# Optimization experiments

Measured on AMD Instinct MI355X. Metric: run time of the kernel, lower is better.

The kernel has to match this reference:

```python
import jax, jax.numpy as jnp
import numpy as np

HID = 64
IN_DIM = 6


def setup_inputs() -> dict:
    key = jax.random.key(0)
    ks = jax.random.split(key, 16)
    B, S, N, D = 8, 32, 64, IN_DIM
    g = lambda k, shape, fan_in: jax.random.normal(k, shape, jnp.float32) / np.sqrt(fan_in)
    return {
        "x": jax.random.normal(ks[0], (B, S, N, D), jnp.float32),
        "emb_w": g(ks[1], (D, HID), D),
        "emb_b": jnp.zeros((HID,), jnp.float32),
        "edge_w1": g(ks[2], (2 * HID + 1, HID), 2 * HID + 1),
        "edge_b1": jnp.zeros((HID,), jnp.float32),
        "edge_w2": g(ks[3], (HID, HID), HID),
        "edge_b2": jnp.zeros((HID,), jnp.float32),
        "node_w1": g(ks[4], (2 * HID, HID), 2 * HID),
        "node_b1": jnp.zeros((HID,), jnp.float32),
        "node_w2": g(ks[5], (HID, HID), HID),
        "node_b2": jnp.zeros((HID,), jnp.float32),
        "coord_w1": g(ks[6], (HID, HID), HID),
        "coord_b1": jnp.zeros((HID,), jnp.float32),
        "coord_w2": g(ks[7], (HID, 1), HID),
        "final_w": g(ks[8], (HID, IN_DIM), HID),
        "final_b": jnp.zeros((IN_DIM,), jnp.float32),
    }


def reference(x, emb_w, emb_b, edge_w1, edge_b1, edge_w2, edge_b2,
              node_w1, node_b1, node_w2, node_b2,
              coord_w1, coord_b1, coord_w2, final_w, final_b):
    B, S, N, D = x.shape
    xf = x.reshape(B * S, N, D)           # [G,N,6]
    pos, vel = xf[..., :3], xf[..., 3:]
    h = xf @ emb_w + emb_b                # [G,N,H]

    rel = pos[:, :, None, :] - pos[:, None, :, :]          # [G,N,N,3]
    dist_sq = jnp.sum(rel * rel, axis=-1, keepdims=True)   # [G,N,N,1]

    H = h.shape[-1]
    h_i = jnp.broadcast_to(h[:, :, None, :], (B * S, N, N, H))
    h_j = jnp.broadcast_to(h[:, None, :, :], (B * S, N, N, H))
    e_in = jnp.concatenate([h_i, h_j, dist_sq], axis=-1)   # [G,N,N,2H+1]
    m_ij = jax.nn.relu(e_in @ edge_w1 + edge_b1) @ edge_w2 + edge_b2  # [G,N,N,H]
    m_i = m_ij.sum(axis=2)                                  # [G,N,H]

    w = jax.nn.relu(m_ij @ coord_w1 + coord_b1) @ coord_w2  # [G,N,N,1]
    pos_out = pos + (rel * w).sum(axis=2) / N

    n_in = jnp.concatenate([h, m_i], axis=-1)
    h = h + jax.nn.relu(n_in @ node_w1 + node_b1) @ node_w2 + node_b2
    vel_out = vel + (h @ final_w + final_b)[..., 3:]

    out = jnp.concatenate([pos_out, vel_out], axis=-1)
    return out.reshape(B, S, N, D)
```

## Files before the change

### kernel.cpp

```cpp
#include <hip/hip_runtime.h>


#define NG 256

typedef __attribute__((ext_vector_type(4))) float f32x4;
typedef __attribute__((ext_vector_type(8))) __bf16 bf16x8;

__device__ __forceinline__ f32x4 mfma16(bf16x8 a, bf16x8 b, f32x4 c){
  return __builtin_amdgcn_mfma_f32_16x16x32_bf16(a, b, c, 0, 0, 0);
}

__device__ __forceinline__ void fma4x4(float* acc, float4 a, float4 b){
  acc[0]  += a.x*b.x; acc[1]  += a.x*b.y; acc[2]  += a.x*b.z; acc[3]  += a.x*b.w;
  acc[4]  += a.y*b.x; acc[5]  += a.y*b.y; acc[6]  += a.y*b.z; acc[7]  += a.y*b.w;
  acc[8]  += a.z*b.x; acc[9]  += a.z*b.y; acc[10] += a.z*b.z; acc[11] += a.z*b.w;
  acc[12] += a.w*b.x; acc[13] += a.w*b.y; acc[14] += a.w*b.z; acc[15] += a.w*b.w;
}

__global__ __launch_bounds__(512, 1)
void egnn_edge_mfma(const float* __restrict__ x,
    const float* __restrict__ emb_w,  const float* __restrict__ emb_b,
    const float* __restrict__ edge_w1,const float* __restrict__ edge_b1,
    const float* __restrict__ edge_w2,const float* __restrict__ edge_b2,
    const float* __restrict__ coord_w1,const float* __restrict__ coord_b1,
    const float* __restrict__ coord_w2,
    float* __restrict__ out, float* __restrict__ ws_mi)
{
  __shared__ __align__(16) float  sAB [64*64];
  __shared__ __align__(16) __bf16 sC  [64*72];
  __shared__ __align__(16) __bf16 sW3t[64*72];
  __shared__ __align__(16) __bf16 sW2t[64*72];
  __shared__ __align__(16) __bf16 sTr [64*72];
  __shared__ float sDsq[8][64];
  __shared__ float sPX[64], sPY[64], sPZ[64];
  __shared__ __align__(16) float sW1L[64];
  __shared__ float sCB1p[64], sCW2[64], sB2[64], sB1[64];
  __shared__ __align__(16) float sW1a[64*64], sW1b[64*64], sW2T[64*64], sCW1[64*64];
  __shared__ __align__(16) float sHt[64*64];
  __shared__ float sXL[384], sEW[384], sEB[64];

  const int bs  = blockIdx.x, tid = threadIdx.x;
  const int lane = tid & 63, wv = tid >> 6;
  const float* xg = x + bs*384;

  if (tid < 384){ sXL[tid] = xg[tid]; sEW[tid] = emb_w[tid]; }
  if (tid < 64){
    sEB[tid] = emb_b[tid];  sB1[tid] = edge_b1[tid]; sB2[tid] = edge_b2[tid];
    sCW2[tid] = coord_w2[tid]; sW1L[tid] = edge_w1[128*64 + tid];
  } else if (tid < 128){
    int j = tid-64; sPX[j]=xg[j*6]; sPY[j]=xg[j*6+1]; sPZ[j]=xg[j*6+2];
  }
  {
    const float4* w1 = (const float4*)edge_w1;
    const float4* cw = (const float4*)coord_w1;
    float4* da=(float4*)sW1a; float4* db=(float4*)sW1b; float4* dc=(float4*)sCW1;
    #pragma unroll
    for (int e=0;e<2;e++){ int q=tid+e*512; da[q]=w1[q]; db[q]=w1[1024+q]; dc[q]=cw[q]; }
  }
  #pragma unroll
  for (int e=0;e<8;e++){ int idx=tid+e*512; int n=idx>>6, k=idx&63;
    sW2T[idx] = edge_w2[k*64+n]; }
  __syncthreads();

  #pragma unroll
  for (int e=0;e<8;e++){
    int idx=tid+e*512; int m=idx>>6, j=idx&63;
    float v = sEB[m];
    #pragma unroll
    for (int d=0;d<6;d++) v += sXL[j*6+d]*sEW[d*64+m];
    sHt[idx] = v;
  }
  __syncthreads();

  const int g = tid>>8, tl = tid&255, tjx = tl>>4, tnx = tl&15;
  {
    float acc[16] = {};
    const float* Bm = g ? sW1b : sW1a;
    #pragma unroll 8
    for (int k=0;k<64;k++){
      float4 av = *(const float4*)&sHt[k*64 + 4*tjx];
      float4 bv = *(const float4*)&Bm [k*64 + 4*tnx];
      fma4x4(acc, av, bv);
    }
    if (g==0){
      #pragma unroll
      for (int r=0;r<4;r++)
        #pragma unroll
        for (int c=0;c<4;c++)
          sAB[(4*tjx+r)*64 + 4*tnx+c] = acc[r*4+c] + sB1[4*tnx+c];
    } else {
      #pragma unroll
      for (int r=0;r<4;r++)
        #pragma unroll
        for (int c=0;c<4;c++)
          sC[(4*tjx+r)*72 + 4*tnx+c] = (__bf16)acc[r*4+c];
    }
  }
  if (g==0){
    float acc[16] = {};
    #pragma unroll 8
    for (int k=0;k<64;k++){
      float4 av = *(const float4*)&sW2T[k*64 + 4*tjx];
      float4 bv = *(const float4*)&sCW1[k*64 + 4*tnx];
      fma4x4(acc, av, bv);
    }
    #pragma unroll
    for (int r=0;r<4;r++)
      #pragma unroll
      for (int c=0;c<4;c++)
        sW3t[(4*tnx+c)*72 + 4*tjx+r] = (__bf16)acc[r*4+c];
  } else {
    #pragma unroll
    for (int e=0;e<16;e++){ int idx=tl+e*256; sW2t[(idx>>6)*72 + (idx&63)] = (__bf16)sW2T[idx]; }
    if (tl < 64){
      float s = coord_b1[tl];
      for (int n=0;n<64;n++) s += sB2[n]*sCW1[n*64+tl];
      sCB1p[tl] = s;
    }
  }
  __syncthreads();

  const int lg = lane>>4, ln = lane&15;

  bf16x8 bW3[4][2];
  #pragma unroll
  for (int nt=0;nt<4;nt++)
    #pragma unroll
    for (int kb=0;kb<2;kb++)
      bW3[nt][kb] = *(const bf16x8*)&sW3t[(nt*16+ln)*72 + kb*32 + lg*8];
  float w18[2][8];
  #pragma unroll
  for (int kb=0;kb<2;kb++){
    *(float4*)&w18[kb][0] = *(const float4*)&sW1L[kb*32+lg*8];
    *(float4*)&w18[kb][4] = *(const float4*)&sW1L[kb*32+lg*8+4];
  }
  float cb1v[4], cw2v[4];
  #pragma unroll
  for (int nt=0;nt<4;nt++){ cb1v[nt]=sCB1p[nt*16+ln]; cw2v[nt]=sCW2[nt*16+ln]; }

  for (int ib=0; ib<8; ib++){
    const int i = ib*8 + wv;
    {
      float dx=sPX[i]-sPX[lane], dy=sPY[i]-sPY[lane], dz=sPZ[i]-sPZ[lane];
      sDsq[wv][lane] = dx*dx+dy*dy+dz*dz;
    }
    float ab8[2][8];
    #pragma unroll
    for (int kb=0;kb<2;kb++){
      *(float4*)&ab8[kb][0] = *(const float4*)&sAB[i*64 + kb*32+lg*8];
      *(float4*)&ab8[kb][4] = *(const float4*)&sAB[i*64 + kb*32+lg*8+4];
    }
    float trs[2][8];
    #pragma unroll
    for (int kb=0;kb<2;kb++)
      #pragma unroll
      for (int e=0;e<8;e++) trs[kb][e]=0.f;

    float sw=0.f, swx=0.f, swy=0.f, swz=0.f;

    #pragma unroll
    for (int jt=0;jt<4;jt++){
      const int j = jt*16 + ln;
      const float dq = sDsq[wv][j];
      f32x4 a4[4];
      #pragma unroll
      for (int nt=0;nt<4;nt++) a4[nt] = f32x4{0.f,0.f,0.f,0.f};

      #pragma unroll
      for (int kb=0;kb<2;kb++){
        bf16x8 c8 = *(const bf16x8*)&sC[j*72 + kb*32 + lg*8];
        bf16x8 t8;
        #pragma unroll
        for (int e=0;e<8;e++){
          float v = ab8[kb][e] + (float)c8[e] + dq*w18[kb][e];
          v = fmaxf(v, 0.f);
          trs[kb][e] += v;
          t8[e] = (__bf16)v;
        }
        #pragma unroll
        for (int nt=0;nt<4;nt++)
          a4[nt] = mfma16(t8, bW3[nt][kb], a4[nt]);
      }

      float wr[4];
      #pragma unroll
      for (int r=0;r<4;r++){
        float p = 0.f;
        #pragma unroll
        for (int nt=0;nt<4;nt++){
          float u = a4[nt][r] + cb1v[nt];
          p += fmaxf(u, 0.f)*cw2v[nt];
        }
        p += __shfl_xor(p,1); p += __shfl_xor(p,2);
        p += __shfl_xor(p,4); p += __shfl_xor(p,8);
        wr[r] = p;
      }
      #pragma unroll
      for (int r=0;r<4;r++){
        int jj = jt*16 + lg*4 + r;
        sw  += wr[r];
        swx += wr[r]*sPX[jj];
        swy += wr[r]*sPY[jj];
        swz += wr[r]*sPZ[jj];
      }
    }

    #pragma unroll
    for (int kb=0;kb<2;kb++)
      #pragma unroll
      for (int e=0;e<8;e++){
        float s = trs[kb][e];
        s += __shfl_xor(s,1); s += __shfl_xor(s,2);
        s += __shfl_xor(s,4); s += __shfl_xor(s,8);
        trs[kb][e] = s;
      }
    if (ln == 0){
      #pragma unroll
      for (int kb=0;kb<2;kb++){
        bf16x8 t8;
        #pragma unroll
        for (int e=0;e<8;e++) t8[e] = (__bf16)trs[kb][e];
        *(bf16x8*)&sTr[i*72 + kb*32 + lg*8] = t8;
      }
    }

    sw  += __shfl_xor(sw,16);  sw  += __shfl_xor(sw,32);
    swx += __shfl_xor(swx,16); swx += __shfl_xor(swx,32);
    swy += __shfl_xor(swy,16); swy += __shfl_xor(swy,32);
    swz += __shfl_xor(swz,16); swz += __shfl_xor(swz,32);
    if (lane == 0){
      float* o = out + (bs*64 + i)*6;
      o[0] = sPX[i] + (sPX[i]*sw - swx)*(1.f/64.f);
      o[1] = sPY[i] + (sPY[i]*sw - swy)*(1.f/64.f);
      o[2] = sPZ[i] + (sPZ[i]*sw - swz)*(1.f/64.f);
    }
  }

  __syncthreads();
  #pragma unroll
  for (int t2=0;t2<2;t2++){
    int t  = wv*2 + t2;
    int it = t>>2, nt = t&3;
    f32x4 a2 = f32x4{0.f,0.f,0.f,0.f};
    #pragma unroll
    for (int kb=0;kb<2;kb++){
      bf16x8 a8 = *(const bf16x8*)&sTr [(it*16+ln)*72 + kb*32 + lg*8];
      bf16x8 b8 = *(const bf16x8*)&sW2t[(nt*16+ln)*72 + kb*32 + lg*8];
      a2 = mfma16(a8, b8, a2);
    }
    int n = nt*16 + ln;
    float b2n = 64.f*sB2[n];
    #pragma unroll
    for (int r=0;r<4;r++){
      int i = it*16 + lg*4 + r;
      ws_mi[(bs*64 + i)*64 + n] = a2[r] + b2n;
    }
  }
}

__global__ __launch_bounds__(256)
void egnn_node_kernel(const float* __restrict__ x,
    const float* __restrict__ emb_w,  const float* __restrict__ emb_b,
    const float* __restrict__ node_w1,const float* __restrict__ node_b1,
    const float* __restrict__ node_w2,const float* __restrict__ node_b2,
    const float* __restrict__ final_w,const float* __restrict__ final_b,
    float* __restrict__ out, const float* __restrict__ ws_mi)
{
  __shared__ __align__(16) float sHt [64*64];
  __shared__ __align__(16) float sMIt[64*68];
  __shared__ __align__(16) float sNW1[128*64];
  __shared__ __align__(16) float sNW2[64*64];
  __shared__ __align__(16) float sZt [64*68];
  __shared__ float sXL[384], sEW[384], sEB[64], sNB1[64], sNB2[64];
  __shared__ float sFW[64*3], sFB[3];

  const int bs = blockIdx.x, tid = threadIdx.x;
  const float* xg = x + bs*64*6;

  for (int q=tid; q<384; q+=256){ sXL[q]=xg[q]; sEW[q]=emb_w[q]; }
  if (tid < 64){ sEB[tid]=emb_b[tid]; sNB1[tid]=node_b1[tid]; sNB2[tid]=node_b2[tid]; }
  if (tid < 192) sFW[tid] = final_w[(tid/3)*6 + 3 + (tid%3)];
  if (tid < 3)   sFB[tid] = final_b[3+tid];
  {
    const float4* g1 = (const float4*)node_w1; float4* d1 = (float4*)sNW1;
    #pragma unroll
    for (int e=0;e<8;e++) d1[tid + e*256] = g1[tid + e*256];
    const float4* g2 = (const float4*)node_w2; float4* d2 = (float4*)sNW2;
    #pragma unroll
    for (int e=0;e<4;e++) d2[tid + e*256] = g2[tid + e*256];
  }
  const float* mig = ws_mi + bs*4096;
  #pragma unroll
  for (int e=0;e<16;e++){
    int idx = tid + e*256; int iN = idx>>6, n = idx&63;
    sMIt[n*68 + iN] = mig[idx];
  }
  __syncthreads();
  #pragma unroll
  for (int e=0;e<16;e++){
    int idx = tid + e*256; int m = idx>>6, j = idx&63;
    float v = sEB[m];
    #pragma unroll
    for (int d=0;d<6;d++) v += sXL[j*6+d]*sEW[d*64+m];
    sHt[idx] = v;
  }
  __syncthreads();

  const int tj = tid>>4, tn = tid&15;
  {
    float acc[16] = {};
    #pragma unroll 8
    for (int k=0;k<64;k++){
      float4 av = *(const float4*)&sHt [k*64 + 4*tj];
      float4 bv = *(const float4*)&sNW1[k*64 + 4*tn];
      fma4x4(acc, av, bv);
    }
    #pragma unroll 8
    for (int k=0;k<64;k++){
      float4 av = *(const float4*)&sMIt[k*68 + 4*tj];
      float4 bv = *(const float4*)&sNW1[(64+k)*64 + 4*tn];
      fma4x4(acc, av, bv);
    }
    #pragma unroll
    for (int c=0;c<4;c++){
      float nb = sNB1[4*tn+c];
      float4 v = make_float4(fmaxf(acc[0+c]+nb,0.f), fmaxf(acc[4+c]+nb,0.f),
                             fmaxf(acc[8+c]+nb,0.f), fmaxf(acc[12+c]+nb,0.f));
      *(float4*)&sZt[(4*tn+c)*68 + 4*tj] = v;
    }
  }
  __syncthreads();
  {
    float acc[16] = {};
    #pragma unroll 8
    for (int k=0;k<64;k++){
      float4 av = *(const float4*)&sZt [k*68 + 4*tj];
      float4 bv = *(const float4*)&sNW2[k*64 + 4*tn];
      fma4x4(acc, av, bv);
    }
    float fv[4][3] = {};
    #pragma unroll
    for (int r=0;r<4;r++){
      #pragma unroll
      for (int c=0;c<4;c++){
        int n = 4*tn+c, j = 4*tj+r;
        float hn = acc[r*4+c] + sHt[n*64 + j] + sNB2[n];
        fv[r][0] += hn*sFW[n*3+0];
        fv[r][1] += hn*sFW[n*3+1];
        fv[r][2] += hn*sFW[n*3+2];
      }
    }
    #pragma unroll
    for (int off=1; off<16; off<<=1){
      #pragma unroll
      for (int r=0;r<4;r++){
        fv[r][0] += __shfl_xor(fv[r][0], off);
        fv[r][1] += __shfl_xor(fv[r][1], off);
        fv[r][2] += __shfl_xor(fv[r][2], off);
      }
    }
    if (tn == 0){
      #pragma unroll
      for (int r=0;r<4;r++){
        int j = 4*tj+r; int base = (bs*64+j)*6;
        #pragma unroll
        for (int d=0;d<3;d++)
          out[base+3+d] = xg[j*6+3+d] + sFB[d] + fv[r][d];
      }
    }
  }
}

extern "C" void kernel_launch(void* const* d_in, const int* in_sizes, int n_in,
                              void* d_out, int out_size, void* d_ws, size_t ws_size,
                              hipStream_t stream)
{
  const float* x        = (const float*)d_in[0];
  const float* emb_w    = (const float*)d_in[1];
  const float* emb_b    = (const float*)d_in[2];
  const float* edge_w1  = (const float*)d_in[3];
  const float* edge_b1  = (const float*)d_in[4];
  const float* edge_w2  = (const float*)d_in[5];
  const float* edge_b2  = (const float*)d_in[6];
  const float* node_w1  = (const float*)d_in[7];
  const float* node_b1  = (const float*)d_in[8];
  const float* node_w2  = (const float*)d_in[9];
  const float* node_b2  = (const float*)d_in[10];
  const float* coord_w1 = (const float*)d_in[11];
  const float* coord_b1 = (const float*)d_in[12];
  const float* coord_w2 = (const float*)d_in[13];
  const float* final_w  = (const float*)d_in[14];
  const float* final_b  = (const float*)d_in[15];
  float* out   = (float*)d_out;
  float* ws_mi = (float*)d_ws;

  egnn_edge_mfma<<<NG, 512, 0, stream>>>(x, emb_w, emb_b,
      edge_w1, edge_b1, edge_w2, edge_b2, coord_w1, coord_b1, coord_w2,
      out, ws_mi);
  egnn_node_kernel<<<NG, 256, 0, stream>>>(x, emb_w, emb_b,
      node_w1, node_b1, node_w2, node_b2, final_w, final_b,
      out, ws_mi);
}
```

Baseline: 86.95 us.

## Rewrite node kernel with bf16 MFMA and fold node_w2 into final projection

The node kernel now runs its first 64x128 GEMM on bf16 MFMA instead of scalar FP32 FMAs. Because only three output columns of the final projection are used, node_w2 is precomposed with final_w (G = W2·Fw) and the hidden-state, bias and residual terms are folded into small vectors. This removes the second 64x64 GEMM entirely. The edge kernel's launch bound is switched to the amdgpu_waves_per_eu attribute. Node-stage inputs are rounded to bf16, which adds a precision risk.

```diff
diff --git a/kernel.cpp b/kernel.cpp
--- a/kernel.cpp
+++ b/kernel.cpp
@@ -17,7 +17,7 @@
   acc[12] += a.w*b.x; acc[13] += a.w*b.y; acc[14] += a.w*b.z; acc[15] += a.w*b.w;
 }
 
-__global__ __launch_bounds__(512, 1)
+__global__ __launch_bounds__(512) __attribute__((amdgpu_waves_per_eu(1)))
 void egnn_edge_mfma(const float* __restrict__ x,
     const float* __restrict__ emb_w,  const float* __restrict__ emb_b,
     const float* __restrict__ edge_w1,const float* __restrict__ edge_b1,
@@ -259,114 +259,108 @@
 }
 
 __global__ __launch_bounds__(256)
-void egnn_node_kernel(const float* __restrict__ x,
+void egnn_node_mfma(const float* __restrict__ x,
     const float* __restrict__ emb_w,  const float* __restrict__ emb_b,
     const float* __restrict__ node_w1,const float* __restrict__ node_b1,
     const float* __restrict__ node_w2,const float* __restrict__ node_b2,
     const float* __restrict__ final_w,const float* __restrict__ final_b,
     float* __restrict__ out, const float* __restrict__ ws_mi)
 {
-  __shared__ __align__(16) float sHt [64*64];
-  __shared__ __align__(16) float sMIt[64*68];
-  __shared__ __align__(16) float sNW1[128*64];
+  __shared__ __align__(16) float  sHt [64*64];
+  __shared__ __align__(16) __bf16 sAb [64*136];
+  __shared__ __align__(16) __bf16 sNW1t[64*136];
   __shared__ __align__(16) float sNW2[64*64];
-  __shared__ __align__(16) float sZt [64*68];
+  __shared__ float sG  [64*4];
+  __shared__ float sHf3[64*4];
+  __shared__ float sFW3[64*4];
+  __shared__ float sCvec[4];
   __shared__ float sXL[384], sEW[384], sEB[64], sNB1[64], sNB2[64];
-  __shared__ float sFW[64*3], sFB[3];
-
-  const int bs = blockIdx.x, tid = threadIdx.x;
-  const float* xg = x + bs*64*6;
-
-  for (int q=tid; q<384; q+=256){ sXL[q]=xg[q]; sEW[q]=emb_w[q]; }
-  if (tid < 64){ sEB[tid]=emb_b[tid]; sNB1[tid]=node_b1[tid]; sNB2[tid]=node_b2[tid]; }
-  if (tid < 192) sFW[tid] = final_w[(tid/3)*6 + 3 + (tid%3)];
-  if (tid < 3)   sFB[tid] = final_b[3+tid];
-  {
-    const float4* g1 = (const float4*)node_w1; float4* d1 = (float4*)sNW1;
-    #pragma unroll
-    for (int e=0;e<8;e++) d1[tid + e*256] = g1[tid + e*256];
-    const float4* g2 = (const float4*)node_w2; float4* d2 = (float4*)sNW2;
-    #pragma unroll
-    for (int e=0;e<4;e++) d2[tid + e*256] = g2[tid + e*256];
-  }
-  const float* mig = ws_mi + bs*4096;
-  #pragma unroll
-  for (int e=0;e<16;e++){
-    int idx = tid + e*256; int iN = idx>>6, n = idx&63;
-    sMIt[n*68 + iN] = mig[idx];
-  }
-  __syncthreads();
-  #pragma unroll
-  for (int e=0;e<16;e++){
-    int idx = tid + e*256; int m = idx>>6, j = idx&63;
-    float v = sEB[m];
-    #pragma unroll
-    for (int d=0;d<6;d++) v += sXL[j*6+d]*sEW[d*64+m];
-    sHt[idx] = v;
-  }
-  __syncthreads();
-
-  const int tj = tid>>4, tn = tid&15;
-  {
-    float acc[16] = {};
-    #pragma unroll 8
-    for (int k=0;k<64;k++){
-      float4 av = *(const float4*)&sHt [k*64 + 4*tj];
-      float4 bv = *(const float4*)&sNW1[k*64 + 4*tn];
-      fma4x4(acc, av, bv);
-    }
-    #pragma unroll 8
-    for (int k=0;k<64;k++){
-      float4 av = *(const float4*)&sMIt[k*68 + 4*tj];
-      float4 bv = *(const float4*)&sNW1[(64+k)*64 + 4*tn];
-      fma4x4(acc, av, bv);
-    }
-    #pragma unroll
-    for (int c=0;c<4;c++){
-      float nb = sNB1[4*tn+c];
-      float4 v = make_float4(fmaxf(acc[0+c]+nb,0.f), fmaxf(acc[4+c]+nb,0.f),
-                             fmaxf(acc[8+c]+nb,0.f), fmaxf(acc[12+c]+nb,0.f));
-      *(float4*)&sZt[(4*tn+c)*68 + 4*tj] = v;
-    }
-  }
-  __syncthreads();
-  {
-    float acc[16] = {};
-    #pragma unroll 8
-    for (int k=0;k<64;k++){
-      float4 av = *(const float4*)&sZt [k*68 + 4*tj];
-      float4 bv = *(const float4*)&sNW2[k*64 + 4*tn];
-      fma4x4(acc, av, bv);
-    }
-    float fv[4][3] = {};
+
+  const int bs=blockIdx.x, tid=threadIdx.x;
+  const int lane=tid&63, wv=tid>>6, ln=lane&15, lg=lane>>4;
+  const float* xg = x + bs*384;
+
+  for (int q=tid;q<384;q+=256){ sXL[q]=xg[q]; sEW[q]=emb_w[q]; }
+  if (tid<64){ sEB[tid]=emb_b[tid]; sNB1[tid]=node_b1[tid]; sNB2[tid]=node_b2[tid]; }
+  if (tid<192){ int n=tid&63, d=tid>>6; sFW3[n*4+d]=final_w[n*6+3+d]; }
+  { const float4* g2=(const float4*)node_w2; float4* d2=(float4*)sNW2;
+    #pragma unroll
+    for (int e=0;e<4;e++) d2[tid+e*256]=g2[tid+e*256]; }
+  #pragma unroll
+  for (int e=0;e<32;e++){ int idx=tid+e*256; int kk=idx>>6, n=idx&63;
+    sNW1t[n*136+kk]=(__bf16)node_w1[idx]; }
+  { const float* mig = ws_mi + bs*4096;
+    #pragma unroll
+    for (int e=0;e<16;e++){ int idx=tid+e*256; int i=idx>>6, n=idx&63;
+      sAb[i*136+64+n]=(__bf16)mig[idx]; } }
+  __syncthreads();
+
+  { int j=tid&63, mb=tid>>6;
+    #pragma unroll
+    for (int mm=0;mm<16;mm++){ int m=mb*16+mm;
+      float v=sEB[m];
+      #pragma unroll
+      for (int d=0;d<6;d++) v+=sXL[j*6+d]*sEW[d*64+m];
+      sHt[m*64+j]=v; sAb[j*136+m]=(__bf16)v; } }
+  __syncthreads();
+
+  if (tid<192){
+    int k=tid&63, d=tid>>6;
+    float gacc=0.f, s=0.f;
+    for (int nn=0;nn<64;nn++){
+      int n=(nn+k)&63;
+      gacc += sNW2[k*64+n]*sFW3[n*4+d];
+      s    += sHt[nn*64+k]*sFW3[nn*4+d];
+    }
+    sG[k*4+d]=gacc; sHf3[k*4+d]=s;
+  } else if (tid<195){
+    int d=tid-192; float c=final_b[3+d];
+    for (int n=0;n<64;n++) c+=sNB2[n]*sFW3[n*4+d];
+    sCvec[d]=c;
+  }
+  __syncthreads();
+
+  f32x4 acc[4];
+  #pragma unroll
+  for (int nt=0;nt<4;nt++) acc[nt]=f32x4{0.f,0.f,0.f,0.f};
+  #pragma unroll
+  for (int kb=0;kb<4;kb++){
+    bf16x8 a8 = *(const bf16x8*)&sAb[(wv*16+ln)*136 + kb*32 + lg*8];
+    #pragma unroll
+    for (int nt=0;nt<4;nt++){
+      bf16x8 b8 = *(const bf16x8*)&sNW1t[(nt*16+ln)*136 + kb*32 + lg*8];
+      acc[nt]=mfma16(a8,b8,acc[nt]);
+    }
+  }
+  float p[4][3];
+  #pragma unroll
+  for(int r=0;r<4;r++){ p[r][0]=0.f; p[r][1]=0.f; p[r][2]=0.f; }
+  #pragma unroll
+  for (int nt=0;nt<4;nt++){
+    int n=nt*16+ln;
+    float zb=sNB1[n];
+    float g0=sG[n*4], g1=sG[n*4+1], g2=sG[n*4+2];
     #pragma unroll
     for (int r=0;r<4;r++){
-      #pragma unroll
-      for (int c=0;c<4;c++){
-        int n = 4*tn+c, j = 4*tj+r;
-        float hn = acc[r*4+c] + sHt[n*64 + j] + sNB2[n];
-        fv[r][0] += hn*sFW[n*3+0];
-        fv[r][1] += hn*sFW[n*3+1];
-        fv[r][2] += hn*sFW[n*3+2];
-      }
-    }
-    #pragma unroll
-    for (int off=1; off<16; off<<=1){
-      #pragma unroll
-      for (int r=0;r<4;r++){
-        fv[r][0] += __shfl_xor(fv[r][0], off);
-        fv[r][1] += __shfl_xor(fv[r][1], off);
-        fv[r][2] += __shfl_xor(fv[r][2], off);
-      }
-    }
-    if (tn == 0){
-      #pragma unroll
-      for (int r=0;r<4;r++){
-        int j = 4*tj+r; int base = (bs*64+j)*6;
-        #pragma unroll
-        for (int d=0;d<3;d++)
-          out[base+3+d] = xg[j*6+3+d] + sFB[d] + fv[r][d];
-      }
+      float u=fmaxf(acc[nt][r]+zb,0.f);
+      p[r][0]+=u*g0; p[r][1]+=u*g1; p[r][2]+=u*g2;
+    }
+  }
+  #pragma unroll
+  for (int off=1;off<16;off<<=1)
+    #pragma unroll
+    for (int r=0;r<4;r++){
+      p[r][0]+=__shfl_xor(p[r][0],off);
+      p[r][1]+=__shfl_xor(p[r][1],off);
+      p[r][2]+=__shfl_xor(p[r][2],off);
+    }
+  if (ln==0){
+    #pragma unroll
+    for (int r=0;r<4;r++){
+      int j=wv*16+lg*4+r; int base=(bs*64+j)*6;
+      #pragma unroll
+      for (int d=0;d<3;d++)
+        out[base+3+d]=xg[j*6+3+d]+sHf3[j*4+d]+sCvec[d]+p[r][d];
     }
   }
 }
@@ -397,7 +391,7 @@
   egnn_edge_mfma<<<NG, 512, 0, stream>>>(x, emb_w, emb_b,
       edge_w1, edge_b1, edge_w2, edge_b2, coord_w1, coord_b1, coord_w2,
       out, ws_mi);
-  egnn_node_kernel<<<NG, 256, 0, stream>>>(x, emb_w, emb_b,
+  egnn_node_mfma<<<NG, 256, 0, stream>>>(x, emb_w, emb_b,
       node_w1, node_b1, node_w2, node_b2, final_w, final_b,
       out, ws_mi);
 }
```

Result: faster. 82.66 us (-4.9%).
